# Kernel optimization log

Hardware: AMD Instinct MI355X
Metric: run time of the kernel (lower is better)

The kernel has to match this reference:

```python
import jax, jax.numpy as jnp
import numpy as np

NA = 10        # num_agents
P = 65536      # num_parallel envs
IN = 16        # input_size
DP = 2         # dim_p
E = 64         # embed_dim = hidden_dim // 2
H = 128        # h_dim


def _uniform(key, shape):
    # torch init: uniform(-stdv, stdv) with stdv = 1/sqrt(last_dim)
    stdv = 1.0 / np.sqrt(shape[-1])
    return jax.random.uniform(key, shape, jnp.float32, -stdv, stdv)


def setup_inputs() -> dict:
    key = jax.random.key(0)
    ks = jax.random.split(key, 8)
    inp = jax.random.normal(ks[0], (NA * P, IN), jnp.float32)
    W_enc = _uniform(ks[1], (IN - DP, E))
    b_enc = jnp.zeros((E,), jnp.float32)
    W_goal = _uniform(ks[2], (DP, E))
    b_goal = jnp.zeros((E,), jnp.float32)
    Wq = _uniform(ks[3], (E, E))   # n_heads=1, key_dim=val_dim=E
    Wk = _uniform(ks[4], (E, E))
    Wv = _uniform(ks[5], (E, E))
    Wo = _uniform(ks[6], (E, E))
    W_upd = _uniform(ks[7], (2 * E, E))
    b_upd = jnp.zeros((E,), jnp.float32)
    return dict(inp=inp, W_enc=W_enc, b_enc=b_enc, W_goal=W_goal, b_goal=b_goal,
                Wq=Wq, Wk=Wk, Wv=Wv, Wo=Wo, W_upd=W_upd, b_upd=b_upd)


def reference(inp, W_enc, b_enc, W_goal, b_goal, Wq, Wk, Wv, Wo, W_upd, b_upd):
    # split agent features / goal
    agent_inp = inp[:, :IN - DP]                     # (NA*P, 14)
    # goal: view(NA, P, DP).transpose(0,1)[:, 0, :] == first P rows' goal cols
    goal = inp[:P, IN - DP:]                         # (P, DP)

    # encoder: Linear + ReLU, then regroup agent-major -> (P, NA, E)
    h = jax.nn.relu(agent_inp @ W_enc + b_enc)
    h = h.reshape(NA, P, E).transpose(1, 0, 2)       # (P, NA, E)

    # single-head attention with custom mask (eye + first column blocked)
    scale = 1.0 / np.sqrt(E)
    Q = h @ Wq                                       # (P, NA, E)
    K = h @ Wk
    V = h @ Wv
    compat = jnp.einsum('bqd,bkd->bqk', Q, K) * scale  # (P, NA, NA)
    mask = jnp.eye(NA, dtype=bool) | (jnp.arange(NA)[None, :] == 0)
    compat = jnp.where(mask[None, :, :], -jnp.inf, compat)
    attn = jax.nn.softmax(compat, axis=-1)
    m = jnp.einsum('bqk,bkd->bqd', attn, V) @ Wo     # (P, NA, E)

    # update MLP on [h, m]
    h1 = jax.nn.relu(jnp.concatenate([h, m], axis=2) @ W_upd + b_upd)  # (P, NA, E)

    # second half: goal embedding for leader, leader's h for followers
    h2_leader = jax.nn.relu(goal @ W_goal + b_goal)[:, None, :]        # (P, 1, E)
    h2_followers = jnp.broadcast_to(h[:, :1, :], (P, NA - 1, E))        # (P, NA-1, E)
    h2 = jnp.concatenate([h2_leader, h2_followers], axis=1)            # (P, NA, E)

    hc = jnp.concatenate([h1, h2], axis=2)           # (P, NA, H)
    h_leader = hc[:, 0, :]                           # (P, H)
    h_followers = hc[:, 1:, :].transpose(1, 0, 2).reshape(-1, H)  # ((NA-1)*P, H)
    return (h_leader, h_followers)
```

## Files before the change

kernel.cpp:

```cpp
#include <hip/hip_runtime.h>
#include <math.h>

#define NAG 10
#define PP  65536
#define EE  64
#define INW 16
#define TP  4
#define RR  (TP*NAG)
#define SH  72
#define SX  40
#define SVT 52
#define SU  68
#define NBLK 1280
#define NGRP (PP/TP)

typedef __attribute__((ext_vector_type(8))) short short8;
typedef __attribute__((ext_vector_type(4))) short short4v;
typedef __attribute__((ext_vector_type(4))) float f32x4;

#if defined(__has_builtin)
#if __has_builtin(__builtin_amdgcn_mfma_f32_16x16x16bf16_1k)
#define HAVE_MFMA16 1
#endif
#endif

__device__ __forceinline__ short f2bf(float x){
    unsigned u = __float_as_uint(x);
    return (short)((u + 0x8000u) >> 16);
}
__device__ __forceinline__ float bf2f(short s){
    return __uint_as_float(((unsigned)(unsigned short)s) << 16);
}
__device__ __forceinline__ unsigned pack2(float a, float b){
    return (unsigned)(unsigned short)f2bf(a) | ((unsigned)(unsigned short)f2bf(b) << 16);
}

__global__ __launch_bounds__(256, 5) void mpnn_mfma4(
    const float* __restrict__ inp,
    const float* __restrict__ W_enc, const float* __restrict__ b_enc,
    const float* __restrict__ W_goal, const float* __restrict__ b_goal,
    const float* __restrict__ Wq, const float* __restrict__ Wk,
    const float* __restrict__ Wv, const float* __restrict__ Wo,
    const float* __restrict__ W_upd, const float* __restrict__ b_upd,
    float* __restrict__ out)
{
    __shared__ __align__(16) char pool[27392];
    __shared__ __align__(16) short Xs[48 * SX];
    __shared__ float goal_s[TP][2];
#ifndef HAVE_MFMA16
    __shared__ float attn_s[TP][NAG][12];
#endif

    short* const hs   = (short*)pool;
    short* const qsb  = hs  + 48*SH;
    short* const ksb  = qsb + 48*SH;
    short* const vsbT = ksb + 48*SH;
    float* const Wc     = (float*)pool;
    float* const outt_u = (float*)(pool + 2*2*48*SH);
    float* const outt_h = (float*)(pool + 2*2*48*SH) + RR*SU;

    const int tid  = threadIdx.x;
    const int w    = tid >> 6;
    const int l    = tid & 63;
    const int lrow = l & 15;
    const int lk   = l >> 4;
    const int col  = 16*w + lrow;

    for (int i = tid; i < 48*SX; i += 256) Xs[i] = 0;

    for (int i = tid; i < EE*EE; i += 256) {
        const int k = i >> 6, n = i & 63;
        float s = 0.f;
        #pragma unroll 8
        for (int d = 0; d < EE; ++d)
            s = fmaf(Wo[k*EE + d], W_upd[(EE + d)*EE + n], s);
        Wc[i] = s;
    }
    __syncthreads();

    short8 fenc, fqw[2], fkw[2], fvw[2], fuw[2], fcw[2];
    #pragma unroll
    for (int j = 0; j < 8; ++j) {
        int k = lk*8 + j;
        fenc[j] = (k < 14) ? f2bf(W_enc[k*EE + col]) : (short)0;
    }
    #pragma unroll
    for (int ks = 0; ks < 2; ++ks) {
        #pragma unroll
        for (int j = 0; j < 8; ++j) {
            int k = 32*ks + lk*8 + j;
            fqw[ks][j] = f2bf(Wq[k*EE + col]);
            fkw[ks][j] = f2bf(Wk[k*EE + col]);
            fvw[ks][j] = f2bf(Wv[k*EE + col]);
            fuw[ks][j] = f2bf(W_upd[k*EE + col]);
            fcw[ks][j] = f2bf(Wc[k*EE + col]);
        }
    }
    const float bencv = b_enc[col];
    const float bupdv = b_upd[col];
    const float wg0 = W_goal[l], wg1 = W_goal[EE + l], bg = b_goal[l];

    const bool hasx = tid < RR*4;
    const int  r_ = tid >> 2, q_ = tid & 3;
    const int  pl_ = r_ / NAG, a_ = r_ - pl_*NAG;
    const size_t xbase = (size_t)a_*PP*INW + (size_t)pl_*INW + (size_t)q_*4;
    f32x4 xin = {0.f,0.f,0.f,0.f};
    if (hasx) xin = __builtin_nontemporal_load(
        (const f32x4*)(inp + xbase + (size_t)blockIdx.x * (TP*INW)));

    if (hasx) {
        uint2 pk = { pack2(xin[0], xin[1]), pack2(xin[2], xin[3]) };
        *(uint2*)&Xs[r_*SX + q_*4] = pk;
        if (q_ == 3 && a_ == 0) { goal_s[pl_][0] = xin[2]; goal_s[pl_][1] = xin[3]; }
        if ((int)blockIdx.x + NBLK < NGRP)
            xin = __builtin_nontemporal_load(
                (const f32x4*)(inp + xbase + (size_t)(blockIdx.x + NBLK) * (TP*INW)));
    }
    __syncthreads();

    for (int g = blockIdx.x; g < NGRP; g += NBLK) {
        const int p0 = g * TP;

        const float h2l = fmaxf(fmaf(goal_s[w][0], wg0,
                           fmaf(goal_s[w][1], wg1, bg)), 0.f);

        #pragma unroll
        for (int rt = 0; rt < 3; ++rt) {
            const short8 ax = *reinterpret_cast<const short8*>(&Xs[(16*rt + lrow)*SX + lk*8]);
            f32x4 acc = {0.f,0.f,0.f,0.f};
            acc = __builtin_amdgcn_mfma_f32_16x16x32_bf16(ax, fenc, acc, 0,0,0);
            #pragma unroll
            for (int j = 0; j < 4; ++j)
                hs[(16*rt + lk*4 + j)*SH + col] = f2bf(fmaxf(acc[j] + bencv, 0.f));
        }
        __syncthreads();

        #pragma unroll
        for (int rt = 0; rt < 3; ++rt) {
            const short8 a0 = *reinterpret_cast<const short8*>(&hs[(16*rt + lrow)*SH + lk*8]);
            const short8 a1 = *reinterpret_cast<const short8*>(&hs[(16*rt + lrow)*SH + 32 + lk*8]);
            f32x4 qa = {0.f,0.f,0.f,0.f}, ka = {0.f,0.f,0.f,0.f}, va = {0.f,0.f,0.f,0.f};
            qa = __builtin_amdgcn_mfma_f32_16x16x32_bf16(a0, fqw[0], qa, 0,0,0);
            qa = __builtin_amdgcn_mfma_f32_16x16x32_bf16(a1, fqw[1], qa, 0,0,0);
            ka = __builtin_amdgcn_mfma_f32_16x16x32_bf16(a0, fkw[0], ka, 0,0,0);
            ka = __builtin_amdgcn_mfma_f32_16x16x32_bf16(a1, fkw[1], ka, 0,0,0);
            va = __builtin_amdgcn_mfma_f32_16x16x32_bf16(a0, fvw[0], va, 0,0,0);
            va = __builtin_amdgcn_mfma_f32_16x16x32_bf16(a1, fvw[1], va, 0,0,0);
            #pragma unroll
            for (int j = 0; j < 4; ++j) {
                const int ro = (16*rt + lk*4 + j)*SH + col;
                qsb[ro] = f2bf(qa[j]);
                ksb[ro] = f2bf(ka[j]);
            }
            uint2 vpk = { pack2(va[0], va[1]), pack2(va[2], va[3]) };
            *(uint2*)&vsbT[col*SVT + 16*rt + lk*4] = vpk;
        }
        const float h0 = bf2f(hs[(w*NAG)*SH + l]);
        __syncthreads();

        {
            const int r0 = w * NAG;
            const short8 aK0 = *reinterpret_cast<const short8*>(&ksb[(r0+lrow)*SH + lk*8]);
            const short8 aK1 = *reinterpret_cast<const short8*>(&ksb[(r0+lrow)*SH + 32 + lk*8]);
            const short8 aQ0 = *reinterpret_cast<const short8*>(&qsb[(r0+lrow)*SH + lk*8]);
            const short8 aQ1 = *reinterpret_cast<const short8*>(&qsb[(r0+lrow)*SH + 32 + lk*8]);
            f32x4 st = {0.f,0.f,0.f,0.f};
            st = __builtin_amdgcn_mfma_f32_16x16x32_bf16(aK0, aQ0, st, 0,0,0);
            st = __builtin_amdgcn_mfma_f32_16x16x32_bf16(aK1, aQ1, st, 0,0,0);
            const int q = lrow;
            float c[4]; float mx4 = -1e30f;
            #pragma unroll
            for (int j = 0; j < 4; ++j) {
                const int k = lk*4 + j;
                const bool valid = (q < NAG) && (k < NAG) && (k != q) && (k != 0);
                c[j] = valid ? st[j] * 0.125f : -1e30f;
                mx4 = fmaxf(mx4, c[j]);
            }
            float mx = fmaxf(mx4, __shfl_xor(mx4, 16, 64));
            mx = fmaxf(mx, __shfl_xor(mx, 32, 64));
            float e[4], s4 = 0.f;
            #pragma unroll
            for (int j = 0; j < 4; ++j) { e[j] = __expf(c[j] - mx); s4 += e[j]; }
            float s = s4;
            s += __shfl_xor(s, 16, 64);
            s += __shfl_xor(s, 32, 64);
            const float inv = 1.f / s;

#ifdef HAVE_MFMA16
            short4v pa;
            #pragma unroll
            for (int j = 0; j < 4; ++j) pa[j] = f2bf(e[j] * inv);
            #pragma unroll
            for (int t = 0; t < 4; ++t) {
                const short* vp = &vsbT[(16*t + lrow)*SVT + r0 + lk*4];
                const unsigned lo = *(const unsigned*)(vp);
                const unsigned hi = *(const unsigned*)(vp + 2);
                short4v vb;
                vb[0] = (short)(lo & 0xffff); vb[1] = (short)(lo >> 16);
                vb[2] = (short)(hi & 0xffff); vb[3] = (short)(hi >> 16);
                f32x4 md = {0.f,0.f,0.f,0.f};
                md = __builtin_amdgcn_mfma_f32_16x16x16bf16_1k(pa, vb, md, 0,0,0);
                #pragma unroll
                for (int j = 0; j < 4; ++j) {
                    const int a = lk*4 + j;
                    if (a < NAG) qsb[(r0+a)*SH + 16*t + lrow] = f2bf(md[j]);
                }
            }
#else
            if (q < NAG) {
                #pragma unroll
                for (int j = 0; j < 4; ++j) {
                    const int k = lk*4 + j;
                    if (k < NAG) attn_s[w][q][k] = e[j] * inv;
                }
            }
            float vv[NAG];
            #pragma unroll
            for (int kk = 0; kk < NAG; ++kk) vv[kk] = bf2f(vsbT[l*SVT + r0 + kk]);
            #pragma unroll
            for (int a = 0; a < NAG; ++a) {
                float m = 0.f;
                #pragma unroll
                for (int kk = 0; kk < NAG; ++kk)
                    m = fmaf(attn_s[w][a][kk], vv[kk], m);
                qsb[(r0+a)*SH + l] = f2bf(m);
            }
#endif
        }
        if (hasx && g + NBLK < NGRP) {
            uint2 pk = { pack2(xin[0], xin[1]), pack2(xin[2], xin[3]) };
            *(uint2*)&Xs[r_*SX + q_*4] = pk;
            if (q_ == 3 && a_ == 0) { goal_s[pl_][0] = xin[2]; goal_s[pl_][1] = xin[3]; }
            if (g + 2*NBLK < NGRP)
                xin = __builtin_nontemporal_load(
                    (const f32x4*)(inp + xbase + (size_t)(g + 2*NBLK) * (TP*INW)));
        }
        __syncthreads();

        #pragma unroll
        for (int rt = 0; rt < 3; ++rt) {
            const short8 a0 = *reinterpret_cast<const short8*>(&hs [(16*rt + lrow)*SH + lk*8]);
            const short8 a1 = *reinterpret_cast<const short8*>(&hs [(16*rt + lrow)*SH + 32 + lk*8]);
            const short8 a2 = *reinterpret_cast<const short8*>(&qsb[(16*rt + lrow)*SH + lk*8]);
            const short8 a3 = *reinterpret_cast<const short8*>(&qsb[(16*rt + lrow)*SH + 32 + lk*8]);
            f32x4 ua = {0.f,0.f,0.f,0.f};
            ua = __builtin_amdgcn_mfma_f32_16x16x32_bf16(a0, fuw[0], ua, 0,0,0);
            ua = __builtin_amdgcn_mfma_f32_16x16x32_bf16(a1, fuw[1], ua, 0,0,0);
            ua = __builtin_amdgcn_mfma_f32_16x16x32_bf16(a2, fcw[0], ua, 0,0,0);
            ua = __builtin_amdgcn_mfma_f32_16x16x32_bf16(a3, fcw[1], ua, 0,0,0);
            #pragma unroll
            for (int j = 0; j < 4; ++j) {
                const int r = 16*rt + lk*4 + j;
                if (r < RR) outt_u[r*SU + col] = fmaxf(ua[j] + bupdv, 0.f);
            }
        }
        outt_h[(w*2 + 0)*64 + l] = h2l;
        outt_h[(w*2 + 1)*64 + l] = h0;
        __syncthreads();

        float* __restrict__ outF = out + (size_t)PP*128;
        #pragma unroll
        for (int it = 0; it < 5; ++it) {
            const int flat   = it*256 + tid;
            const int a      = flat >> 7;
            const int within = flat & 127;
            const int pl     = within >> 5;
            const int j4     = within & 31;
            const float* src = (j4 < 16)
                ? &outt_u[(pl*NAG + a)*SU + j4*4]
                : &outt_h[(pl*2 + (a == 0 ? 0 : 1))*64 + (j4 - 16)*4];
            const f32x4 v = *reinterpret_cast<const f32x4*>(src);
            float* dst = (a == 0)
                ? (out  + ((size_t)(p0 + pl))*128 + j4*4)
                : (outF + ((size_t)(a-1)*PP + (size_t)(p0 + pl))*128 + j4*4);
            __builtin_nontemporal_store(v, (f32x4*)dst);
        }
    }
}

extern "C" void kernel_launch(void* const* d_in, const int* in_sizes, int n_in,
                              void* d_out, int out_size, void* d_ws, size_t ws_size,
                              hipStream_t stream) {
    const float* inp    = (const float*)d_in[0];
    const float* W_enc  = (const float*)d_in[1];
    const float* b_enc  = (const float*)d_in[2];
    const float* W_goal = (const float*)d_in[3];
    const float* b_goal = (const float*)d_in[4];
    const float* Wq     = (const float*)d_in[5];
    const float* Wk     = (const float*)d_in[6];
    const float* Wv     = (const float*)d_in[7];
    const float* Wo     = (const float*)d_in[8];
    const float* W_upd  = (const float*)d_in[9];
    const float* b_upd  = (const float*)d_in[10];

    hipLaunchKernelGGL(mpnn_mfma4, dim3(NBLK), dim3(256), 0, stream,
                       inp, W_enc, b_enc, W_goal, b_goal,
                       Wq, Wk, Wv, Wo, W_upd, b_upd, (float*)d_out);
}
```

Before: 261.5 us.

## Fold Wq·Wkᵀ and Wv·Wo·W_upd into precomputed weights to cut per-tile GEMMs

Precomputes Wq·Wkᵀ (scaled) and Wv·(Wo·W_upd_bottom) per block, so each tile computes G=h·Wqk and Z=h·Wvc instead of separate Q, K, V projections and the message-update GEMM. Scores become h·Gᵀ, and the attention output is already projected, so it is added directly to the h·W_upd_top accumulator. This removes MFMAs and shared-memory buffers, which lets LDS shrink, occupancy rise to 6 blocks and the grid grow. In exchange it adds a larger per-block weight precompute, an extra barrier per iteration, plain loads replacing nontemporal input loads, and different bf16 rounding.

Result: slower. 457.2 us (+74.8%).

```diff
diff --git a/kernel.cpp b/kernel.cpp
--- a/kernel.cpp
+++ b/kernel.cpp
@@ -9,21 +9,15 @@
 #define RR  (TP*NAG)
 #define SH  72
 #define SX  40
-#define SVT 52
+#define SZT 52
 #define SU  68
-#define NBLK 1280
+#define NBLK 1536
 #define NGRP (PP/TP)
 
 typedef __attribute__((ext_vector_type(8))) short short8;
 typedef __attribute__((ext_vector_type(4))) short short4v;
 typedef __attribute__((ext_vector_type(4))) float f32x4;
 
-#if defined(__has_builtin)
-#if __has_builtin(__builtin_amdgcn_mfma_f32_16x16x16bf16_1k)
-#define HAVE_MFMA16 1
-#endif
-#endif
-
 __device__ __forceinline__ short f2bf(float x){
     unsigned u = __float_as_uint(x);
     return (short)((u + 0x8000u) >> 16);
@@ -35,7 +29,7 @@
     return (unsigned)(unsigned short)f2bf(a) | ((unsigned)(unsigned short)f2bf(b) << 16);
 }
 
-__global__ __launch_bounds__(256, 5) void mpnn_mfma4(
+__global__ __launch_bounds__(256, 6) void mpnn_mfma5(
     const float* __restrict__ inp,
     const float* __restrict__ W_enc, const float* __restrict__ b_enc,
     const float* __restrict__ W_goal, const float* __restrict__ b_goal,
@@ -44,20 +38,16 @@
     const float* __restrict__ W_upd, const float* __restrict__ b_upd,
     float* __restrict__ out)
 {
-    __shared__ __align__(16) char pool[27392];
+    __shared__ __align__(16) char pool[20480];
     __shared__ __align__(16) short Xs[48 * SX];
     __shared__ float goal_s[TP][2];
-#ifndef HAVE_MFMA16
-    __shared__ float attn_s[TP][NAG][12];
-#endif
 
     short* const hs   = (short*)pool;
-    short* const qsb  = hs  + 48*SH;
-    short* const ksb  = qsb + 48*SH;
-    short* const vsbT = ksb + 48*SH;
-    float* const Wc     = (float*)pool;
-    float* const outt_u = (float*)(pool + 2*2*48*SH);
-    float* const outt_h = (float*)(pool + 2*2*48*SH) + RR*SU;
+    short* const gsb  = hs  + 48*SH;
+    short* const zsbT = gsb + 48*SH;
+    float* const Wf     = (float*)pool;
+    float* const outt_u = (float*)gsb;
+    float* const outt_h = outt_u + RR*SU;
 
     const int tid  = threadIdx.x;
     const int w    = tid >> 6;
@@ -69,33 +59,57 @@
     for (int i = tid; i < 48*SX; i += 256) Xs[i] = 0;
 
     for (int i = tid; i < EE*EE; i += 256) {
-        const int k = i >> 6, n = i & 63;
+        const int r = i >> 6, c = i & 63;
+        float s = 0.f;
+        #pragma unroll 8
+        for (int t = 0; t < EE; ++t)
+            s = fmaf(Wq[r*EE + t], Wk[c*EE + t], s);
+        Wf[i] = s * 0.125f;
+    }
+    __syncthreads();
+
+    short8 fqk[2];
+    #pragma unroll
+    for (int ks = 0; ks < 2; ++ks)
+        #pragma unroll
+        for (int j = 0; j < 8; ++j)
+            fqk[ks][j] = f2bf(Wf[(32*ks + lk*8 + j)*EE + col]);
+    __syncthreads();
+
+    for (int i = tid; i < EE*EE; i += 256) {
+        const int r = i >> 6, c = i & 63;
         float s = 0.f;
         #pragma unroll 8
         for (int d = 0; d < EE; ++d)
-            s = fmaf(Wo[k*EE + d], W_upd[(EE + d)*EE + n], s);
-        Wc[i] = s;
-    }
-    __syncthreads();
-
-    short8 fenc, fqw[2], fkw[2], fvw[2], fuw[2], fcw[2];
+            s = fmaf(Wo[r*EE + d], W_upd[(EE + d)*EE + c], s);
+        Wf[i] = s;
+    }
+    __syncthreads();
+
+    short8 fvc[2];
+    #pragma unroll
+    for (int ks = 0; ks < 2; ++ks)
+        #pragma unroll
+        for (int j = 0; j < 8; ++j) {
+            const int k = 32*ks + lk*8 + j;
+            float s = 0.f;
+            #pragma unroll 8
+            for (int d = 0; d < EE; ++d)
+                s = fmaf(Wv[k*EE + d], Wf[d*EE + col], s);
+            fvc[ks][j] = f2bf(s);
+        }
+
+    short8 fenc, fuw[2];
     #pragma unroll
     for (int j = 0; j < 8; ++j) {
         int k = lk*8 + j;
         fenc[j] = (k < 14) ? f2bf(W_enc[k*EE + col]) : (short)0;
     }
     #pragma unroll
-    for (int ks = 0; ks < 2; ++ks) {
-        #pragma unroll
-        for (int j = 0; j < 8; ++j) {
-            int k = 32*ks + lk*8 + j;
-            fqw[ks][j] = f2bf(Wq[k*EE + col]);
-            fkw[ks][j] = f2bf(Wk[k*EE + col]);
-            fvw[ks][j] = f2bf(Wv[k*EE + col]);
-            fuw[ks][j] = f2bf(W_upd[k*EE + col]);
-            fcw[ks][j] = f2bf(Wc[k*EE + col]);
-        }
-    }
+    for (int ks = 0; ks < 2; ++ks)
+        #pragma unroll
+        for (int j = 0; j < 8; ++j)
+            fuw[ks][j] = f2bf(W_upd[(32*ks + lk*8 + j)*EE + col]);
     const float bencv = b_enc[col];
     const float bupdv = b_upd[col];
     const float wg0 = W_goal[l], wg1 = W_goal[EE + l], bg = b_goal[l];
@@ -105,16 +119,14 @@
     const int  pl_ = r_ / NAG, a_ = r_ - pl_*NAG;
     const size_t xbase = (size_t)a_*PP*INW + (size_t)pl_*INW + (size_t)q_*4;
     f32x4 xin = {0.f,0.f,0.f,0.f};
-    if (hasx) xin = __builtin_nontemporal_load(
-        (const f32x4*)(inp + xbase + (size_t)blockIdx.x * (TP*INW)));
+    if (hasx) xin = *(const f32x4*)(inp + xbase + (size_t)blockIdx.x * (TP*INW));
 
     if (hasx) {
         uint2 pk = { pack2(xin[0], xin[1]), pack2(xin[2], xin[3]) };
         *(uint2*)&Xs[r_*SX + q_*4] = pk;
         if (q_ == 3 && a_ == 0) { goal_s[pl_][0] = xin[2]; goal_s[pl_][1] = xin[3]; }
         if ((int)blockIdx.x + NBLK < NGRP)
-            xin = __builtin_nontemporal_load(
-                (const f32x4*)(inp + xbase + (size_t)(blockIdx.x + NBLK) * (TP*INW)));
+            xin = *(const f32x4*)(inp + xbase + (size_t)(blockIdx.x + NBLK) * (TP*INW));
     }
     __syncthreads();
 
@@ -139,41 +151,36 @@
         for (int rt = 0; rt < 3; ++rt) {
             const short8 a0 = *reinterpret_cast<const short8*>(&hs[(16*rt + lrow)*SH + lk*8]);
             const short8 a1 = *reinterpret_cast<const short8*>(&hs[(16*rt + lrow)*SH + 32 + lk*8]);
-            f32x4 qa = {0.f,0.f,0.f,0.f}, ka = {0.f,0.f,0.f,0.f}, va = {0.f,0.f,0.f,0.f};
-            qa = __builtin_amdgcn_mfma_f32_16x16x32_bf16(a0, fqw[0], qa, 0,0,0);
-            qa = __builtin_amdgcn_mfma_f32_16x16x32_bf16(a1, fqw[1], qa, 0,0,0);
-            ka = __builtin_amdgcn_mfma_f32_16x16x32_bf16(a0, fkw[0], ka, 0,0,0);
-            ka = __builtin_amdgcn_mfma_f32_16x16x32_bf16(a1, fkw[1], ka, 0,0,0);
-            va = __builtin_amdgcn_mfma_f32_16x16x32_bf16(a0, fvw[0], va, 0,0,0);
-            va = __builtin_amdgcn_mfma_f32_16x16x32_bf16(a1, fvw[1], va, 0,0,0);
-            #pragma unroll
-            for (int j = 0; j < 4; ++j) {
-                const int ro = (16*rt + lk*4 + j)*SH + col;
-                qsb[ro] = f2bf(qa[j]);
-                ksb[ro] = f2bf(ka[j]);
-            }
-            uint2 vpk = { pack2(va[0], va[1]), pack2(va[2], va[3]) };
-            *(uint2*)&vsbT[col*SVT + 16*rt + lk*4] = vpk;
+            f32x4 ga = {0.f,0.f,0.f,0.f}, za = {0.f,0.f,0.f,0.f};
+            ga = __builtin_amdgcn_mfma_f32_16x16x32_bf16(a0, fqk[0], ga, 0,0,0);
+            ga = __builtin_amdgcn_mfma_f32_16x16x32_bf16(a1, fqk[1], ga, 0,0,0);
+            za = __builtin_amdgcn_mfma_f32_16x16x32_bf16(a0, fvc[0], za, 0,0,0);
+            za = __builtin_amdgcn_mfma_f32_16x16x32_bf16(a1, fvc[1], za, 0,0,0);
+            #pragma unroll
+            for (int j = 0; j < 4; ++j)
+                gsb[(16*rt + lk*4 + j)*SH + col] = f2bf(ga[j]);
+            uint2 zpk = { pack2(za[0], za[1]), pack2(za[2], za[3]) };
+            *(uint2*)&zsbT[col*SZT + 16*rt + lk*4] = zpk;
         }
         const float h0 = bf2f(hs[(w*NAG)*SH + l]);
         __syncthreads();
 
         {
             const int r0 = w * NAG;
-            const short8 aK0 = *reinterpret_cast<const short8*>(&ksb[(r0+lrow)*SH + lk*8]);
-            const short8 aK1 = *reinterpret_cast<const short8*>(&ksb[(r0+lrow)*SH + 32 + lk*8]);
-            const short8 aQ0 = *reinterpret_cast<const short8*>(&qsb[(r0+lrow)*SH + lk*8]);
-            const short8 aQ1 = *reinterpret_cast<const short8*>(&qsb[(r0+lrow)*SH + 32 + lk*8]);
+            const short8 aH0 = *reinterpret_cast<const short8*>(&hs [(r0+lrow)*SH + lk*8]);
+            const short8 aH1 = *reinterpret_cast<const short8*>(&hs [(r0+lrow)*SH + 32 + lk*8]);
+            const short8 aG0 = *reinterpret_cast<const short8*>(&gsb[(r0+lrow)*SH + lk*8]);
+            const short8 aG1 = *reinterpret_cast<const short8*>(&gsb[(r0+lrow)*SH + 32 + lk*8]);
             f32x4 st = {0.f,0.f,0.f,0.f};
-            st = __builtin_amdgcn_mfma_f32_16x16x32_bf16(aK0, aQ0, st, 0,0,0);
-            st = __builtin_amdgcn_mfma_f32_16x16x32_bf16(aK1, aQ1, st, 0,0,0);
+            st = __builtin_amdgcn_mfma_f32_16x16x32_bf16(aH0, aG0, st, 0,0,0);
+            st = __builtin_amdgcn_mfma_f32_16x16x32_bf16(aH1, aG1, st, 0,0,0);
             const int q = lrow;
             float c[4]; float mx4 = -1e30f;
             #pragma unroll
             for (int j = 0; j < 4; ++j) {
                 const int k = lk*4 + j;
                 const bool valid = (q < NAG) && (k < NAG) && (k != q) && (k != 0);
-                c[j] = valid ? st[j] * 0.125f : -1e30f;
+                c[j] = valid ? st[j] : -1e30f;
                 mx4 = fmaxf(mx4, c[j]);
             }
             float mx = fmaxf(mx4, __shfl_xor(mx4, 16, 64));
@@ -186,13 +193,12 @@
             s += __shfl_xor(s, 32, 64);
             const float inv = 1.f / s;
 
-#ifdef HAVE_MFMA16
             short4v pa;
             #pragma unroll
             for (int j = 0; j < 4; ++j) pa[j] = f2bf(e[j] * inv);
             #pragma unroll
             for (int t = 0; t < 4; ++t) {
-                const short* vp = &vsbT[(16*t + lrow)*SVT + r0 + lk*4];
+                const short* vp = &zsbT[(16*t + lrow)*SZT + r0 + lk*4];
                 const unsigned lo = *(const unsigned*)(vp);
                 const unsigned hi = *(const unsigned*)(vp + 2);
                 short4v vb;
@@ -203,55 +209,40 @@
                 #pragma unroll
                 for (int j = 0; j < 4; ++j) {
                     const int a = lk*4 + j;
-                    if (a < NAG) qsb[(r0+a)*SH + 16*t + lrow] = f2bf(md[j]);
+                    if (a < NAG) gsb[(r0+a)*SH + 16*t + lrow] = f2bf(md[j]);
                 }
             }
-#else
-            if (q < NAG) {
-                #pragma unroll
-                for (int j = 0; j < 4; ++j) {
-                    const int k = lk*4 + j;
-                    if (k < NAG) attn_s[w][q][k] = e[j] * inv;
-                }
-            }
-            float vv[NAG];
-            #pragma unroll
-            for (int kk = 0; kk < NAG; ++kk) vv[kk] = bf2f(vsbT[l*SVT + r0 + kk]);
-            #pragma unroll
-            for (int a = 0; a < NAG; ++a) {
-                float m = 0.f;
-                #pragma unroll
-                for (int kk = 0; kk < NAG; ++kk)
-                    m = fmaf(attn_s[w][a][kk], vv[kk], m);
-                qsb[(r0+a)*SH + l] = f2bf(m);
-            }
-#endif
         }
         if (hasx && g + NBLK < NGRP) {
             uint2 pk = { pack2(xin[0], xin[1]), pack2(xin[2], xin[3]) };
             *(uint2*)&Xs[r_*SX + q_*4] = pk;
             if (q_ == 3 && a_ == 0) { goal_s[pl_][0] = xin[2]; goal_s[pl_][1] = xin[3]; }
             if (g + 2*NBLK < NGRP)
-                xin = __builtin_nontemporal_load(
-                    (const f32x4*)(inp + xbase + (size_t)(g + 2*NBLK) * (TP*INW)));
-        }
-        __syncthreads();
-
-        #pragma unroll
-        for (int rt = 0; rt < 3; ++rt) {
-            const short8 a0 = *reinterpret_cast<const short8*>(&hs [(16*rt + lrow)*SH + lk*8]);
-            const short8 a1 = *reinterpret_cast<const short8*>(&hs [(16*rt + lrow)*SH + 32 + lk*8]);
-            const short8 a2 = *reinterpret_cast<const short8*>(&qsb[(16*rt + lrow)*SH + lk*8]);
-            const short8 a3 = *reinterpret_cast<const short8*>(&qsb[(16*rt + lrow)*SH + 32 + lk*8]);
+                xin = *(const f32x4*)(inp + xbase + (size_t)(g + 2*NBLK) * (TP*INW));
+        }
+        __syncthreads();
+
+        f32x4 uacc[3];
+        #pragma unroll
+        for (int rt = 0; rt < 3; ++rt) {
+            const short8 a0 = *reinterpret_cast<const short8*>(&hs[(16*rt + lrow)*SH + lk*8]);
+            const short8 a1 = *reinterpret_cast<const short8*>(&hs[(16*rt + lrow)*SH + 32 + lk*8]);
             f32x4 ua = {0.f,0.f,0.f,0.f};
             ua = __builtin_amdgcn_mfma_f32_16x16x32_bf16(a0, fuw[0], ua, 0,0,0);
             ua = __builtin_amdgcn_mfma_f32_16x16x32_bf16(a1, fuw[1], ua, 0,0,0);
-            ua = __builtin_amdgcn_mfma_f32_16x16x32_bf16(a2, fcw[0], ua, 0,0,0);
-            ua = __builtin_amdgcn_mfma_f32_16x16x32_bf16(a3, fcw[1], ua, 0,0,0);
+            #pragma unroll
+            for (int j = 0; j < 4; ++j)
+                ua[j] += bf2f(gsb[(16*rt + lk*4 + j)*SH + col]);
+            uacc[rt] = ua;
+        }
+        __syncthreads();
+
+        #pragma unroll
+        for (int rt = 0; rt < 3; ++rt) {
             #pragma unroll
             for (int j = 0; j < 4; ++j) {
                 const int r = 16*rt + lk*4 + j;
-                if (r < RR) outt_u[r*SU + col] = fmaxf(ua[j] + bupdv, 0.f);
+                if (r < RR) outt_u[r*SU + col] = fmaxf(uacc[rt][j] + bupdv, 0.f);
             }
         }
         outt_h[(w*2 + 0)*64 + l] = h2l;
@@ -275,6 +266,7 @@
                 : (outF + ((size_t)(a-1)*PP + (size_t)(p0 + pl))*128 + j4*4);
             __builtin_nontemporal_store(v, (f32x4*)dst);
         }
+        __syncthreads();
     }
 }
 
@@ -293,7 +285,7 @@
     const float* W_upd  = (const float*)d_in[9];
     const float* b_upd  = (const float*)d_in[10];
 
-    hipLaunchKernelGGL(mpnn_mfma4, dim3(NBLK), dim3(256), 0, stream,
+    hipLaunchKernelGGL(mpnn_mfma5, dim3(NBLK), dim3(256), 0, stream,
                        inp, W_enc, b_enc, W_goal, b_goal,
                        Wq, Wk, Wv, Wo, W_upd, b_upd, (float*)d_out);
 }
```
